# Optimization experiments

Hardware: AMD Instinct MI355X
Metric: run time of the kernel (lower is better)

## Reference

```python
import jax, jax.numpy as jnp
import numpy as np


def setup_inputs() -> dict:
    key = jax.random.key(0)
    k1, k2 = jax.random.split(key)
    B, C, H, W = 4, 128, 256, 448
    feat1 = jax.random.normal(k1, (B, C, H, W), dtype=jnp.float32)
    feat2 = jax.random.normal(k2, (B, C, H, W), dtype=jnp.float32)
    return {"feat1": feat1, "feat2": feat2, "max_disp": 4}


def reference(feat1, feat2, max_disp):
    # PWC-Net cost volume: kernel_size=1, stride1=stride2=1.
    # cost[b, s, h, w] = mean_c feat1[b,c,h,w] * feat2_pad[b,c,h+i,w+j]
    # where s enumerates (i, j) in [0, 2*max_disp]^2, row-major (matching
    # the torch nested i/j loop + cat order).
    B, C, H, W = feat1.shape
    md = int(max_disp)
    num_shifts = 2 * md + 1
    feat2_pad = jnp.pad(feat2, ((0, 0), (0, 0), (md, md), (md, md)))

    ij = jnp.arange(num_shifts)
    offsets = jnp.stack(jnp.meshgrid(ij, ij, indexing="ij"), axis=-1).reshape(-1, 2)  # (S*S, 2)

    def one_shift(off):
        sl = jax.lax.dynamic_slice(feat2_pad, (0, 0, off[0], off[1]), (B, C, H, W))
        return jnp.mean(feat1 * sl, axis=1)  # (B, H, W)

    cost = jax.vmap(one_shift)(offsets)        # (81, B, H, W)
    return jnp.transpose(cost, (1, 0, 2, 3))   # (B, 81, H, W)
```

## Files before the change

### kernel.cpp

```cpp
#include <hip/hip_runtime.h>


typedef __attribute__((ext_vector_type(4))) float f32x4;

__device__ __forceinline__ float bperm(int idx, float v) {
    return __int_as_float(__builtin_amdgcn_ds_bpermute(idx, __float_as_int(v)));
}

__global__ __launch_bounds__(256, 4) void cv_kernel(
    const float* __restrict__ feat1,
    const float* __restrict__ feat2,
    float* __restrict__ out)
{
    constexpr int C = 128, H = 256, W = 448;
    constexpr unsigned HW = (unsigned)(H * W);

    const int tid  = threadIdx.x;
    const int wid  = tid >> 6;
    const int lane = tid & 63;

    const int swz  = (blockIdx.x & 7) * 288 + (blockIdx.x >> 3);
    const int item = swz * 4 + wid;
    const int di   = item % 9;
    const int bh   = item / 9;
    const int h    = bh & 255;
    const int b    = bh >> 8;

    const int m   = (lane < 56) ? lane : 55;
    const int px0 = m << 3;
    const int hr  = h + di - 4;

    float* ob = out + (((size_t)(b * 81 + di * 9)) * H + h) * W + px0;

    if (hr < 0 || hr >= H) {
        if (lane < 56) {
            const f32x4 z = {0.f, 0.f, 0.f, 0.f};
#pragma unroll
            for (int dj = 0; dj < 9; ++dj) {
                *(f32x4*)(ob + (size_t)dj * HW)     = z;
                *(f32x4*)(ob + (size_t)dj * HW + 4) = z;
            }
        }
        return;
    }

    unsigned f1o = (unsigned)(((b * C * H) + h) * W + px0);
    unsigned f2o = (unsigned)(((b * C * H) + hr) * W + px0);

    const int idxL = ((lane - 1) & 63) << 2;
    const int idxR = ((lane + 1) & 63) << 2;

    float acc[9][8];
#pragma unroll
    for (int j = 0; j < 9; ++j)
#pragma unroll
        for (int p = 0; p < 8; ++p) acc[j][p] = 0.0f;

    f32x4 ca0 = *(const f32x4*)(feat1 + f1o);
    f32x4 ca1 = *(const f32x4*)(feat1 + f1o + 4);
    f32x4 cb0 = *(const f32x4*)(feat2 + f2o);
    f32x4 cb1 = *(const f32x4*)(feat2 + f2o + 4);
    f1o += HW; f2o += HW;

    for (int t = 0; t < C - 1; ++t) {
        const f32x4 na0 = *(const f32x4*)(feat1 + f1o);
        const f32x4 na1 = *(const f32x4*)(feat1 + f1o + 4);
        const f32x4 nb0 = *(const f32x4*)(feat2 + f2o);
        const f32x4 nb1 = *(const f32x4*)(feat2 + f2o + 4);
        f1o += HW; f2o += HW;

        const float w[16] = {
            bperm(idxL, cb1.x), bperm(idxL, cb1.y), bperm(idxL, cb1.z), bperm(idxL, cb1.w),
            cb0.x, cb0.y, cb0.z, cb0.w, cb1.x, cb1.y, cb1.z, cb1.w,
            bperm(idxR, cb0.x), bperm(idxR, cb0.y), bperm(idxR, cb0.z), bperm(idxR, cb0.w)};
        const float a[8] = {ca0.x, ca0.y, ca0.z, ca0.w, ca1.x, ca1.y, ca1.z, ca1.w};
#pragma unroll
        for (int dj = 0; dj < 9; ++dj)
#pragma unroll
            for (int p = 0; p < 8; ++p)
                acc[dj][p] = fmaf(a[p], w[dj + p], acc[dj][p]);

        ca0 = na0; ca1 = na1; cb0 = nb0; cb1 = nb1;
    }
    {
        const float w[16] = {
            bperm(idxL, cb1.x), bperm(idxL, cb1.y), bperm(idxL, cb1.z), bperm(idxL, cb1.w),
            cb0.x, cb0.y, cb0.z, cb0.w, cb1.x, cb1.y, cb1.z, cb1.w,
            bperm(idxR, cb0.x), bperm(idxR, cb0.y), bperm(idxR, cb0.z), bperm(idxR, cb0.w)};
        const float a[8] = {ca0.x, ca0.y, ca0.z, ca0.w, ca1.x, ca1.y, ca1.z, ca1.w};
#pragma unroll
        for (int dj = 0; dj < 9; ++dj)
#pragma unroll
            for (int p = 0; p < 8; ++p)
                acc[dj][p] = fmaf(a[p], w[dj + p], acc[dj][p]);
    }

    if (lane < 56) {
        const float s = 1.0f / 128.0f;
#pragma unroll
        for (int dj = 0; dj < 9; ++dj) {
            float o[8];
#pragma unroll
            for (int p = 0; p < 8; ++p) {
                float v = acc[dj][p] * s;
                if (dj + p < 4)  v = (m == 0)  ? 0.f : v;
                if (dj + p > 11) v = (m == 55) ? 0.f : v;
                o[p] = v;
            }
            f32x4 o0 = {o[0], o[1], o[2], o[3]};
            f32x4 o1 = {o[4], o[5], o[6], o[7]};
            *(f32x4*)(ob + (size_t)dj * HW)     = o0;
            *(f32x4*)(ob + (size_t)dj * HW + 4) = o1;
        }
    }
}

extern "C" void kernel_launch(void* const* d_in, const int* in_sizes, int n_in,
                              void* d_out, int out_size, void* d_ws, size_t ws_size,
                              hipStream_t stream) {
    const float* feat1 = (const float*)d_in[0];
    const float* feat2 = (const float*)d_in[1];
    float* out = (float*)d_out;
    cv_kernel<<<dim3(2304), dim3(256), 0, stream>>>(feat1, feat2, out);
}
```

Baseline: 299.9 us.

## Split each row into two half-row waves with 4 pixels per lane

Each wavefront now covers half a row (56 lanes × 4 pixels) instead of a full row at 8 pixels per lane, which doubles the grid size. Spare lanes 56-57 load halo pixels from the neighbouring half so the lane-shift permutes still supply the left and right neighbours. Accumulators drop from 72 to 36 registers, which is meant to allow more waves per CU and hide load latency. In exchange, global loads and bpermutes per output pixel increase, and the feat1/feat2 row data is fetched twice per half-row.

```diff
diff --git a/kernel.cpp b/kernel.cpp
--- a/kernel.cpp
+++ b/kernel.cpp
@@ -19,98 +19,98 @@
     const int wid  = tid >> 6;
     const int lane = tid & 63;
 
-    const int swz  = (blockIdx.x & 7) * 288 + (blockIdx.x >> 3);
-    const int item = swz * 4 + wid;
-    const int di   = item % 9;
-    const int bh   = item / 9;
-    const int h    = bh & 255;
-    const int b    = bh >> 8;
+    const int swz   = (blockIdx.x & 7) * 576 + (blockIdx.x >> 3);
+    const int item2 = swz * 4 + wid;
+    const int half  = item2 & 1;
+    const int item  = item2 >> 1;
+    const int di    = item % 9;
+    const int bh    = item / 9;
+    const int h     = bh & 255;
+    const int b     = bh >> 8;
 
-    const int m   = (lane < 56) ? lane : 55;
-    const int px0 = m << 3;
-    const int hr  = h + di - 4;
+    const int mg = (lane < 56) ? lane : 55;
+    const int G  = half * 56 + mg;
+    const int hr = h + di - 4;
 
-    float* ob = out + (((size_t)(b * 81 + di * 9)) * H + h) * W + px0;
+    float* ob = out + (((size_t)(b * 81 + di * 9)) * H + h) * W + G * 4;
 
     if (hr < 0 || hr >= H) {
         if (lane < 56) {
             const f32x4 z = {0.f, 0.f, 0.f, 0.f};
 #pragma unroll
-            for (int dj = 0; dj < 9; ++dj) {
-                *(f32x4*)(ob + (size_t)dj * HW)     = z;
-                *(f32x4*)(ob + (size_t)dj * HW + 4) = z;
-            }
+            for (int dj = 0; dj < 9; ++dj)
+                *(f32x4*)(ob + (size_t)dj * HW) = z;
         }
         return;
     }
 
-    unsigned f1o = (unsigned)(((b * C * H) + h) * W + px0);
-    unsigned f2o = (unsigned)(((b * C * H) + hr) * W + px0);
+    int gload;
+    if (half == 0) gload = (lane < 56) ? lane : (lane == 56 ? 56 : (lane == 57 ? 0 : 55));
+    else           gload = (lane < 56) ? 56 + lane : (lane == 56 ? 111 : (lane == 57 ? 55 : 60));
 
-    const int idxL = ((lane - 1) & 63) << 2;
-    const int idxR = ((lane + 1) & 63) << 2;
+    unsigned f1o = (unsigned)(((b * C * H) + h) * W + gload * 4);
+    unsigned f2o = (unsigned)(((b * C * H) + hr) * W + gload * 4);
 
-    float acc[9][8];
+    const int idxL = ((lane == 0)  ? 57 : lane - 1) << 2;
+    const int idxR = ((lane == 55) ? 56 : lane + 1) << 2;
+
+    float acc[9][4];
 #pragma unroll
     for (int j = 0; j < 9; ++j)
 #pragma unroll
-        for (int p = 0; p < 8; ++p) acc[j][p] = 0.0f;
+        for (int p = 0; p < 4; ++p) acc[j][p] = 0.0f;
 
-    f32x4 ca0 = *(const f32x4*)(feat1 + f1o);
-    f32x4 ca1 = *(const f32x4*)(feat1 + f1o + 4);
-    f32x4 cb0 = *(const f32x4*)(feat2 + f2o);
-    f32x4 cb1 = *(const f32x4*)(feat2 + f2o + 4);
+    f32x4 ca = *(const f32x4*)(feat1 + f1o);
+    f32x4 cb = *(const f32x4*)(feat2 + f2o);
     f1o += HW; f2o += HW;
 
     for (int t = 0; t < C - 1; ++t) {
-        const f32x4 na0 = *(const f32x4*)(feat1 + f1o);
-        const f32x4 na1 = *(const f32x4*)(feat1 + f1o + 4);
-        const f32x4 nb0 = *(const f32x4*)(feat2 + f2o);
-        const f32x4 nb1 = *(const f32x4*)(feat2 + f2o + 4);
+        const f32x4 na = *(const f32x4*)(feat1 + f1o);
+        const f32x4 nb = *(const f32x4*)(feat2 + f2o);
         f1o += HW; f2o += HW;
 
-        const float w[16] = {
-            bperm(idxL, cb1.x), bperm(idxL, cb1.y), bperm(idxL, cb1.z), bperm(idxL, cb1.w),
-            cb0.x, cb0.y, cb0.z, cb0.w, cb1.x, cb1.y, cb1.z, cb1.w,
-            bperm(idxR, cb0.x), bperm(idxR, cb0.y), bperm(idxR, cb0.z), bperm(idxR, cb0.w)};
-        const float a[8] = {ca0.x, ca0.y, ca0.z, ca0.w, ca1.x, ca1.y, ca1.z, ca1.w};
+        const float w[12] = {
+            bperm(idxL, cb.x), bperm(idxL, cb.y), bperm(idxL, cb.z), bperm(idxL, cb.w),
+            cb.x, cb.y, cb.z, cb.w,
+            bperm(idxR, cb.x), bperm(idxR, cb.y), bperm(idxR, cb.z), bperm(idxR, cb.w)};
+        const float a[4] = {ca.x, ca.y, ca.z, ca.w};
 #pragma unroll
         for (int dj = 0; dj < 9; ++dj)
 #pragma unroll
-            for (int p = 0; p < 8; ++p)
+            for (int p = 0; p < 4; ++p)
                 acc[dj][p] = fmaf(a[p], w[dj + p], acc[dj][p]);
 
-        ca0 = na0; ca1 = na1; cb0 = nb0; cb1 = nb1;
+        ca = na; cb = nb;
     }
     {
-        const float w[16] = {
-            bperm(idxL, cb1.x), bperm(idxL, cb1.y), bperm(idxL, cb1.z), bperm(idxL, cb1.w),
-            cb0.x, cb0.y, cb0.z, cb0.w, cb1.x, cb1.y, cb1.z, cb1.w,
-            bperm(idxR, cb0.x), bperm(idxR, cb0.y), bperm(idxR, cb0.z), bperm(idxR, cb0.w)};
-        const float a[8] = {ca0.x, ca0.y, ca0.z, ca0.w, ca1.x, ca1.y, ca1.z, ca1.w};
+        const float w[12] = {
+            bperm(idxL, cb.x), bperm(idxL, cb.y), bperm(idxL, cb.z), bperm(idxL, cb.w),
+            cb.x, cb.y, cb.z, cb.w,
+            bperm(idxR, cb.x), bperm(idxR, cb.y), bperm(idxR, cb.z), bperm(idxR, cb.w)};
+        const float a[4] = {ca.x, ca.y, ca.z, ca.w};
 #pragma unroll
         for (int dj = 0; dj < 9; ++dj)
 #pragma unroll
-            for (int p = 0; p < 8; ++p)
+            for (int p = 0; p < 4; ++p)
                 acc[dj][p] = fmaf(a[p], w[dj + p], acc[dj][p]);
     }
 
     if (lane < 56) {
         const float s = 1.0f / 128.0f;
+        const bool leftEdge  = (G == 0);
+        const bool rightEdge = (G == 111);
 #pragma unroll
         for (int dj = 0; dj < 9; ++dj) {
-            float o[8];
+            float o[4];
 #pragma unroll
-            for (int p = 0; p < 8; ++p) {
+            for (int p = 0; p < 4; ++p) {
                 float v = acc[dj][p] * s;
-                if (dj + p < 4)  v = (m == 0)  ? 0.f : v;
-                if (dj + p > 11) v = (m == 55) ? 0.f : v;
+                if (dj + p < 4) v = leftEdge  ? 0.f : v;
+                if (dj + p > 7) v = rightEdge ? 0.f : v;
                 o[p] = v;
             }
-            f32x4 o0 = {o[0], o[1], o[2], o[3]};
-            f32x4 o1 = {o[4], o[5], o[6], o[7]};
-            *(f32x4*)(ob + (size_t)dj * HW)     = o0;
-            *(f32x4*)(ob + (size_t)dj * HW + 4) = o1;
+            f32x4 ov = {o[0], o[1], o[2], o[3]};
+            *(f32x4*)(ob + (size_t)dj * HW) = ov;
         }
     }
 }
@@ -121,5 +121,5 @@
     const float* feat1 = (const float*)d_in[0];
     const float* feat2 = (const float*)d_in[1];
     float* out = (float*)d_out;
-    cv_kernel<<<dim3(2304), dim3(256), 0, stream>>>(feat1, feat2, out);
+    cv_kernel<<<dim3(4608), dim3(256), 0, stream>>>(feat1, feat2, out);
 }
```

After: 320.3 us. 1.07x slower.
